# Performance work log

Hardware: AMD Instinct MI355X
Metric: run time of the kernel (lower is better)

The kernel has to match this reference:

```python
import jax, jax.numpy as jnp
import numpy as np

SL, BS, D = 2048, 2, 1024
H, DH = 16, 64  # num_heads, nhid

def setup_inputs() -> dict:
    key = jax.random.key(0)
    ks = jax.random.split(key, 8)
    inv = 1.0 / np.sqrt(D)
    return {
        "query": jax.random.normal(ks[0], (SL, BS, D), jnp.float32),
        "keys": jax.random.normal(ks[1], (SL, BS, D), jnp.float32),
        "values": jax.random.normal(ks[2], (SL, BS, D), jnp.float32),
        "mask": jnp.ones((1, 1, SL, SL), jnp.int32),
        "Wq": jax.random.normal(ks[3], (H * DH, D), jnp.float32) * inv,
        "Wk": jax.random.normal(ks[4], (H * DH, D), jnp.float32) * inv,
        "Wv": jax.random.normal(ks[5], (H * DH, D), jnp.float32) * inv,
        "Wo": jax.random.normal(ks[6], (D, H * DH), jnp.float32) * inv,
    }

def reference(query, keys, values, mask, Wq, Wk, Wv, Wo):
    slq, bs, _ = query.shape
    sl = keys.shape[0]
    # nn.Linear(bias=False): x @ W.T ; then view to (s, b, H, DH)
    q = (query @ Wq.T).reshape(slq, bs, H, DH)   # sbhd
    k = (keys @ Wk.T).reshape(sl, bs, H, DH)
    v = (values @ Wv.T).reshape(sl, bs, H, DH)
    # NOTE: original forward never applies self.scale -> unscaled scores.
    scores = jnp.einsum('qbhd,kbhd->bhqk', q, k)
    scores = jnp.where(mask == 0, jnp.float32(-1e20), scores)
    weights = jax.nn.softmax(scores, axis=-1)
    attn = jnp.einsum('bhqk,kbhd->qbhd', weights, v).reshape(slq, bs, H * DH)
    return attn @ Wo.T  # [slq, bs, out_dim]
```

## Files before the change

kernel.cpp:

```cpp
#include <hip/hip_runtime.h>


typedef __attribute__((ext_vector_type(4))) float  f32x4;
typedef __attribute__((ext_vector_type(8))) __bf16 bf16x8;
typedef __attribute__((ext_vector_type(4))) __bf16 bf16x4;

#define SLEN 2048
#define BSZ  2
#define DMODEL 1024
#define NHEAD 16
#define DHEAD 64
#define D3 (3 * DMODEL)

__device__ __forceinline__ void async16(void* lds, const void* g) {
    __builtin_amdgcn_global_load_lds(
        (const __attribute__((address_space(1))) unsigned int*)g,
        (__attribute__((address_space(3))) unsigned int*)lds, 16, 0, 0);
}

__device__ __forceinline__ f32x4 mfma16(bf16x8 a, bf16x8 b, f32x4 c) {
    return __builtin_amdgcn_mfma_f32_16x16x32_bf16(a, b, c, 0, 0, 0);
}

struct CvtArgs {
    const float* src[7];
    __bf16* dst[7];
    int n4[7];
    float scale[7];
    const int* mask;
    unsigned int* flag;
    int maskn4;
};
__global__ void cvt_all(CvtArgs a) {
    const int t = blockIdx.y;
    const int stride = gridDim.x * blockDim.x;
    if (t == 7) {
        bool ok = true;
        for (int i = blockIdx.x * blockDim.x + threadIdx.x; i < a.maskn4; i += stride) {
            int4 v = ((const int4*)a.mask)[i];
            ok = ok && v.x && v.y && v.z && v.w;
        }
        if (!ok) atomicAnd(a.flag, 0u);
        return;
    }
    const float* __restrict__ src = a.src[t];
    __bf16* __restrict__ dst = a.dst[t];
    const int n4 = a.n4[t];
    const float sc = a.scale[t];
    for (int i = blockIdx.x * blockDim.x + threadIdx.x; i < n4; i += stride) {
        float4 v = ((const float4*)src)[i];
        bf16x4 o;
        o[0] = (__bf16)(v.x * sc); o[1] = (__bf16)(v.y * sc);
        o[2] = (__bf16)(v.z * sc); o[3] = (__bf16)(v.w * sc);
        ((bf16x4*)dst)[i] = o;
    }
}

template <typename CT>
__device__ __forceinline__ void gemm_core(const char* Ab, const char* Bb, int K,
                                          CT* Cv, size_t crow0, size_t ccol0,
                                          size_t ldc) {
    __shared__ __bf16 At[2][128 * 64];
    __shared__ __bf16 Bt[2][64 * 64];
    const int tid = threadIdx.x;
    const int lane = tid & 63, wv = tid >> 6;
    const int l15 = lane & 15, l4 = lane >> 4;
    const int wr = wv >> 1, wc = wv & 1;
    const int srow = lane >> 3;
    const int sbyte = (((lane & 7) ^ srow) << 4);

    f32x4 acc[4][2];
#pragma unroll
    for (int m = 0; m < 4; m++)
#pragma unroll
        for (int n = 0; n < 2; n++)
#pragma unroll
            for (int r = 0; r < 4; r++) acc[m][n][r] = 0.0f;

    auto stage = [&](int buf, int k0) {
#pragma unroll
        for (int i = 0; i < 6; i++) {
            int c = wv * 6 + i;
            if (c < 16) {
                int row = c * 8 + srow;
                async16(&At[buf][c * 512], Ab + ((size_t)row * K + k0) * 2 + sbyte);
            } else {
                int row = (c - 16) * 8 + srow;
                async16(&Bt[buf][(c - 16) * 512], Bb + ((size_t)row * K + k0) * 2 + sbyte);
            }
        }
    };

    stage(0, 0);
    __syncthreads();
    int cur = 0;
    for (int k0 = 0; k0 < K; k0 += 64) {
        if (k0 + 64 < K) stage(cur ^ 1, k0 + 64);
#pragma unroll
        for (int kk = 0; kk < 2; kk++) {
            bf16x8 af[4], bfr[2];
#pragma unroll
            for (int m = 0; m < 4; m++) {
                int row = wr * 64 + m * 16 + l15;
                int col = (kk * 32 + l4 * 8) ^ ((row & 7) << 3);
                af[m] = *(const bf16x8*)&At[cur][row * 64 + col];
            }
#pragma unroll
            for (int n = 0; n < 2; n++) {
                int row = wc * 32 + n * 16 + l15;
                int col = (kk * 32 + l4 * 8) ^ ((row & 7) << 3);
                bfr[n] = *(const bf16x8*)&Bt[cur][row * 64 + col];
            }
#pragma unroll
            for (int m = 0; m < 4; m++)
#pragma unroll
                for (int n = 0; n < 2; n++)
                    acc[m][n] = mfma16(af[m], bfr[n], acc[m][n]);
        }
        __syncthreads();
        cur ^= 1;
    }

#pragma unroll
    for (int m = 0; m < 4; m++)
#pragma unroll
        for (int n = 0; n < 2; n++)
#pragma unroll
            for (int r = 0; r < 4; r++) {
                size_t row = crow0 + wr * 64 + m * 16 + l4 * 4 + r;
                size_t col = ccol0 + wc * 32 + n * 16 + l15;
                Cv[row * ldc + col] = (CT)acc[m][n][r];
            }
}

__global__ __launch_bounds__(256, 2) void gemm_qkv(const __bf16* __restrict__ Xq,
                                                   const __bf16* __restrict__ Xk,
                                                   const __bf16* __restrict__ Xv,
                                                   const __bf16* __restrict__ W,
                                                   __bf16* __restrict__ C) {
    const int i = blockIdx.x;
    const int swz = (i & 7) * 192 + (i >> 3);
    const int bn = swz / 32, bm = swz % 32;
    const __bf16* A = (bn < 16) ? Xq : (bn < 32) ? Xk : Xv;
    gemm_core<__bf16>((const char*)(A + (size_t)bm * 128 * DMODEL),
                      (const char*)(W + (size_t)bn * 64 * DMODEL), DMODEL,
                      C, (size_t)bm * 128, (size_t)bn * 64, D3);
}

__global__ __launch_bounds__(256, 2) void gemm_out(const __bf16* __restrict__ A,
                                                   const __bf16* __restrict__ B,
                                                   float* __restrict__ Cv) {
    const int i = blockIdx.x;
    const int swz = (i & 7) * 64 + (i >> 3);
    const int bn = swz / 32, bm = swz % 32;
    gemm_core<float>((const char*)(A + (size_t)bm * 128 * DMODEL),
                     (const char*)(B + (size_t)bn * 64 * DMODEL), DMODEL,
                     Cv, (size_t)bm * 128, (size_t)bn * 64, DMODEL);
}

__global__ __launch_bounds__(256) void transpose_v(const __bf16* __restrict__ QKV,
                                                   __bf16* __restrict__ Vt) {
    __shared__ __bf16 t[64][72];
    const int stile = blockIdx.x;
    const int bh = blockIdx.y;
    const int b = bh >> 4, h = bh & 15;
    const int tid = threadIdx.x;
    {
        int sr = tid >> 2, d0 = (tid & 3) * 16;
        const __bf16* src = QKV + ((size_t)((stile * 64 + sr) * BSZ + b) * D3 + 2 * DMODEL + h * 64 + d0);
        *(bf16x8*)&t[sr][d0]     = *(const bf16x8*)src;
        *(bf16x8*)&t[sr][d0 + 8] = *(const bf16x8*)(src + 8);
    }
    __syncthreads();
    {
        int d = tid >> 2, s0 = (tid & 3) * 16;
        bf16x8 o1, o2;
#pragma unroll
        for (int j = 0; j < 8; j++) { o1[j] = t[s0 + j][d]; o2[j] = t[s0 + 8 + j][d]; }
        __bf16* dst = Vt + ((size_t)(bh * 64 + d) * SLEN + stile * 64 + s0);
        *(bf16x8*)dst = o1;
        *(bf16x8*)(dst + 8) = o2;
    }
}

__global__ __launch_bounds__(256, 2) void attn_fwd(const __bf16* __restrict__ QKV,
                                                   const __bf16* __restrict__ Vt,
                                                   const int* __restrict__ mask,
                                                   const unsigned int* __restrict__ flag,
                                                   __bf16* __restrict__ Attn) {
    __shared__ __bf16 Kt[2][2][64 * 64];
    __shared__ __bf16 Vs[2][2][64 * 64];
    __shared__ __bf16 Ps[128 * 64];
    const int tid = threadIdx.x;
    const int lane = tid & 63, wv = tid >> 6;
    const int l15 = lane & 15, l4 = lane >> 4;
    const int blk = blockIdx.x;
    const int xcd = blk & 7, idx = blk >> 3;
    const int bh = xcd + (idx >> 4) * 8;
    const int qt = idx & 15;
    const int b = bh >> 4, h = bh & 15;
    const bool allones = (*flag != 0u);
    const int srow = lane >> 3;
    const int sbyte = (((lane & 7) ^ srow) << 4);

    bf16x8 aq[2][2];
#pragma unroll
    for (int m = 0; m < 2; m++)
#pragma unroll
        for (int kk = 0; kk < 2; kk++) {
            int qrow = qt * 128 + wv * 32 + m * 16 + l15;
            aq[m][kk] = *(const bf16x8*)(QKV + ((size_t)(qrow * BSZ + b) * D3 + h * 64 + kk * 32 + l4 * 8));
        }

    f32x4 o[2][4], lr[2];
#pragma unroll
    for (int m = 0; m < 2; m++) {
#pragma unroll
        for (int nd = 0; nd < 4; nd++)
#pragma unroll
            for (int r = 0; r < 4; r++) o[m][nd][r] = 0.0f;
#pragma unroll
        for (int r = 0; r < 4; r++) lr[m][r] = 0.0f;
    }

    const char* Kb = (const char*)QKV + ((size_t)b * D3 + DMODEL + h * 64) * 2;
    const char* Vb = (const char*)Vt + ((size_t)bh * 64) * SLEN * 2;

    auto stage = [&](int buf, int kt) {
#pragma unroll
        for (int i = 0; i < 8; i++) {
            int c = wv * 8 + i;
            if (c < 16) {
                int kh = c >> 3, ck = c & 7;
                int krow = kt * 128 + kh * 64 + ck * 8 + srow;
                async16(&Kt[buf][kh][ck * 512],
                        Kb + (size_t)krow * (BSZ * D3 * 2) + sbyte);
            } else {
                int c2 = c - 16;
                int kh = c2 >> 3, ck = c2 & 7;
                int drow = ck * 8 + srow;
                async16(&Vs[buf][kh][ck * 512],
                        Vb + (size_t)drow * (SLEN * 2) + kt * 256 + kh * 128 + sbyte);
            }
        }
    };

    stage(0, 0);
    __syncthreads();
    int cur = 0;

    for (int kt = 0; kt < SLEN / 128; kt++) {
        if (kt + 1 < SLEN / 128) stage(cur ^ 1, kt + 1);

#pragma unroll
        for (int kh = 0; kh < 2; kh++) {
            const __bf16* Kl = Kt[cur][kh];
            const __bf16* Vl = Vs[cur][kh];

            f32x4 s[2][4];
#pragma unroll
            for (int m = 0; m < 2; m++)
#pragma unroll
                for (int n = 0; n < 4; n++)
#pragma unroll
                    for (int r = 0; r < 4; r++) s[m][n][r] = 0.0f;
            __builtin_amdgcn_s_setprio(1);
#pragma unroll
            for (int n = 0; n < 4; n++) {
                int row = n * 16 + l15;
#pragma unroll
                for (int kk = 0; kk < 2; kk++) {
                    int col = (kk * 32 + l4 * 8) ^ ((row & 7) << 3);
                    bf16x8 bk = *(const bf16x8*)&Kl[row * 64 + col];
#pragma unroll
                    for (int m = 0; m < 2; m++)
                        s[m][n] = mfma16(aq[m][kk], bk, s[m][n]);
                }
            }
            __builtin_amdgcn_s_setprio(0);

            if (!allones) {
#pragma unroll
                for (int m = 0; m < 2; m++)
#pragma unroll
                    for (int n = 0; n < 4; n++)
#pragma unroll
                        for (int r = 0; r < 4; r++) {
                            int q = qt * 128 + wv * 32 + m * 16 + l4 * 4 + r;
                            int kg = kt * 128 + kh * 64 + n * 16 + l15;
                            if (mask[(size_t)q * SLEN + kg] == 0) s[m][n][r] = -1e20f;
                        }
            }

#pragma unroll
            for (int m = 0; m < 2; m++)
#pragma unroll
                for (int n = 0; n < 4; n++)
#pragma unroll
                    for (int r = 0; r < 4; r++) {
                        float p = __builtin_amdgcn_exp2f(s[m][n][r]);
                        lr[m][r] += p;
                        int row = wv * 32 + m * 16 + l4 * 4 + r;
                        int col = (n * 16 + l15) ^ ((row & 7) << 3);
                        Ps[row * 64 + col] = (__bf16)p;
                    }

            __builtin_amdgcn_s_setprio(1);
#pragma unroll
            for (int ks = 0; ks < 2; ks++) {
                bf16x8 ap[2];
#pragma unroll
                for (int m = 0; m < 2; m++) {
                    int prow = wv * 32 + m * 16 + l15;
                    int pcol = (ks * 32 + l4 * 8) ^ ((prow & 7) << 3);
                    ap[m] = *(const bf16x8*)&Ps[prow * 64 + pcol];
                }
#pragma unroll
                for (int nd = 0; nd < 4; nd++) {
                    int vrow = nd * 16 + l15;
                    int vcol = (ks * 32 + l4 * 8) ^ ((vrow & 7) << 3);
                    bf16x8 bv = *(const bf16x8*)&Vl[vrow * 64 + vcol];
#pragma unroll
                    for (int m = 0; m < 2; m++)
                        o[m][nd] = mfma16(ap[m], bv, o[m][nd]);
                }
            }
            __builtin_amdgcn_s_setprio(0);
        }

        __syncthreads();
        cur ^= 1;
    }

#pragma unroll
    for (int d = 1; d < 16; d <<= 1)
#pragma unroll
        for (int m = 0; m < 2; m++)
#pragma unroll
            for (int r = 0; r < 4; r++) lr[m][r] += __shfl_xor(lr[m][r], d);

#pragma unroll
    for (int m = 0; m < 2; m++) {
        f32x4 inv;
#pragma unroll
        for (int r = 0; r < 4; r++) inv[r] = 1.0f / lr[m][r];
#pragma unroll
        for (int nd = 0; nd < 4; nd++)
#pragma unroll
            for (int r = 0; r < 4; r++) {
                int qrow = qt * 128 + wv * 32 + m * 16 + l4 * 4 + r;
                Attn[((size_t)(qrow * BSZ + b)) * DMODEL + h * 64 + nd * 16 + l15] =
                    (__bf16)(o[m][nd][r] * inv[r]);
            }
    }
}

extern "C" void kernel_launch(void* const* d_in, const int* in_sizes, int n_in,
                              void* d_out, int out_size, void* d_ws, size_t ws_size,
                              hipStream_t stream) {
    const float* query  = (const float*)d_in[0];
    const float* keys   = (const float*)d_in[1];
    const float* values = (const float*)d_in[2];
    const int*   mask   = (const int*)d_in[3];
    const float* Wq     = (const float*)d_in[4];
    const float* Wk     = (const float*)d_in[5];
    const float* Wv     = (const float*)d_in[6];
    const float* Wo     = (const float*)d_in[7];
    float* out = (float*)d_out;

    char* ws = (char*)d_ws;
    const size_t MB = 1024 * 1024;
    __bf16* XQ   = (__bf16*)(ws + 0);
    __bf16* XK   = (__bf16*)(ws + 8 * MB);
    __bf16* XV   = (__bf16*)(ws + 16 * MB);
    __bf16* WCAT = (__bf16*)(ws + 24 * MB);
    __bf16* WQB  = WCAT;
    __bf16* WKB  = (__bf16*)(ws + 26 * MB);
    __bf16* WVB  = (__bf16*)(ws + 28 * MB);
    __bf16* WOB  = (__bf16*)(ws + 30 * MB);
    __bf16* QKV  = (__bf16*)(ws + 32 * MB);
    __bf16* VT   = (__bf16*)(ws + 0);
    __bf16* ATT  = (__bf16*)(ws + 8 * MB);
    unsigned int* flag = (unsigned int*)(ws + 56 * MB);

    (void)hipMemsetAsync(flag, 0xFF, 4, stream);

    const int NTOK = SLEN * BSZ;
    const int NBIG = NTOK * DMODEL / 4, NW = DMODEL * DMODEL / 4;
    const float LOG2E = 1.4426950408889634f;
    CvtArgs ca;
    ca.src[0] = query;  ca.dst[0] = XQ;  ca.n4[0] = NBIG; ca.scale[0] = 1.0f;
    ca.src[1] = keys;   ca.dst[1] = XK;  ca.n4[1] = NBIG; ca.scale[1] = 1.0f;
    ca.src[2] = values; ca.dst[2] = XV;  ca.n4[2] = NBIG; ca.scale[2] = 1.0f;
    ca.src[3] = Wq;     ca.dst[3] = WQB; ca.n4[3] = NW;   ca.scale[3] = LOG2E;
    ca.src[4] = Wk;     ca.dst[4] = WKB; ca.n4[4] = NW;   ca.scale[4] = 1.0f;
    ca.src[5] = Wv;     ca.dst[5] = WVB; ca.n4[5] = NW;   ca.scale[5] = 1.0f;
    ca.src[6] = Wo;     ca.dst[6] = WOB; ca.n4[6] = NW;   ca.scale[6] = 1.0f;
    ca.mask = mask; ca.flag = flag; ca.maskn4 = SLEN * SLEN / 4;
    cvt_all<<<dim3(256, 8), 256, 0, stream>>>(ca);

    gemm_qkv<<<1536, 256, 0, stream>>>(XQ, XK, XV, WCAT, QKV);

    transpose_v<<<dim3(SLEN / 64, BSZ * NHEAD), 256, 0, stream>>>(QKV, VT);

    attn_fwd<<<BSZ * NHEAD * (SLEN / 128), 256, 0, stream>>>(QKV, VT, mask, flag, ATT);

    gemm_out<<<512, 256, 0, stream>>>(ATT, WOB, out);
}
```

Before: 143.8 us.

## Keep softmax probabilities in registers via transposed QK^T and 16x16x16 MFMA for PV

The attention kernel swaps the QK^T MFMA operands so each lane holds scores for one query row across four keys. That lets the exp2 outputs feed a 16x16x16 bf16 MFMA directly as the B operand, so the shared-memory P buffer and its store/load round-trip are gone. Row-sum reductions shrink to two shuffles, output writes become 4-wide vectors, and K fragments are loaded up front. The change also drops the XCD-aware block swizzle in both GEMMs in favour of a plain 2D grid, which may hurt L2 locality. The PV product now issues twice as many smaller-K MFMAs.

```diff
diff --git a/kernel.cpp b/kernel.cpp
--- a/kernel.cpp
+++ b/kernel.cpp
@@ -4,6 +4,7 @@
 typedef __attribute__((ext_vector_type(4))) float  f32x4;
 typedef __attribute__((ext_vector_type(8))) __bf16 bf16x8;
 typedef __attribute__((ext_vector_type(4))) __bf16 bf16x4;
+typedef __attribute__((ext_vector_type(4))) short  s16x4;
 
 #define SLEN 2048
 #define BSZ  2
@@ -20,6 +21,15 @@
 
 __device__ __forceinline__ f32x4 mfma16(bf16x8 a, bf16x8 b, f32x4 c) {
     return __builtin_amdgcn_mfma_f32_16x16x32_bf16(a, b, c, 0, 0, 0);
+}
+
+__device__ __forceinline__ f32x4 mfma16k16(bf16x4 a, bf16x4 b, f32x4 c) {
+#if __has_builtin(__builtin_amdgcn_mfma_f32_16x16x16_bf16)
+    return __builtin_amdgcn_mfma_f32_16x16x16_bf16(a, b, c, 0, 0, 0);
+#else
+    return __builtin_amdgcn_mfma_f32_16x16x16bf16_1k(
+        __builtin_bit_cast(s16x4, a), __builtin_bit_cast(s16x4, b), c, 0, 0, 0);
+#endif
 }
 
 struct CvtArgs {
@@ -138,9 +148,7 @@
                                                    const __bf16* __restrict__ Xv,
                                                    const __bf16* __restrict__ W,
                                                    __bf16* __restrict__ C) {
-    const int i = blockIdx.x;
-    const int swz = (i & 7) * 192 + (i >> 3);
-    const int bn = swz / 32, bm = swz % 32;
+    const int bm = blockIdx.x, bn = blockIdx.y;
     const __bf16* A = (bn < 16) ? Xq : (bn < 32) ? Xk : Xv;
     gemm_core<__bf16>((const char*)(A + (size_t)bm * 128 * DMODEL),
                       (const char*)(W + (size_t)bn * 64 * DMODEL), DMODEL,
@@ -150,9 +158,7 @@
 __global__ __launch_bounds__(256, 2) void gemm_out(const __bf16* __restrict__ A,
                                                    const __bf16* __restrict__ B,
                                                    float* __restrict__ Cv) {
-    const int i = blockIdx.x;
-    const int swz = (i & 7) * 64 + (i >> 3);
-    const int bn = swz / 32, bm = swz % 32;
+    const int bm = blockIdx.x, bn = blockIdx.y;
     gemm_core<float>((const char*)(A + (size_t)bm * 128 * DMODEL),
                      (const char*)(B + (size_t)bn * 64 * DMODEL), DMODEL,
                      Cv, (size_t)bm * 128, (size_t)bn * 64, DMODEL);
@@ -190,7 +196,6 @@
                                                    __bf16* __restrict__ Attn) {
     __shared__ __bf16 Kt[2][2][64 * 64];
     __shared__ __bf16 Vs[2][2][64 * 64];
-    __shared__ __bf16 Ps[128 * 64];
     const int tid = threadIdx.x;
     const int lane = tid & 63, wv = tid >> 6;
     const int l15 = lane & 15, l4 = lane >> 4;
@@ -212,15 +217,15 @@
             aq[m][kk] = *(const bf16x8*)(QKV + ((size_t)(qrow * BSZ + b) * D3 + h * 64 + kk * 32 + l4 * 8));
         }
 
-    f32x4 o[2][4], lr[2];
+    f32x4 o[2][4];
+    float lr[2];
 #pragma unroll
     for (int m = 0; m < 2; m++) {
 #pragma unroll
         for (int nd = 0; nd < 4; nd++)
 #pragma unroll
             for (int r = 0; r < 4; r++) o[m][nd][r] = 0.0f;
-#pragma unroll
-        for (int r = 0; r < 4; r++) lr[m][r] = 0.0f;
+        lr[m] = 0.0f;
     }
 
     const char* Kb = (const char*)QKV + ((size_t)b * D3 + DMODEL + h * 64) * 2;
@@ -257,6 +262,17 @@
             const __bf16* Kl = Kt[cur][kh];
             const __bf16* Vl = Vs[cur][kh];
 
+            bf16x8 bk[4][2];
+#pragma unroll
+            for (int n = 0; n < 4; n++) {
+                int row = n * 16 + l15;
+#pragma unroll
+                for (int kk = 0; kk < 2; kk++) {
+                    int col = (kk * 32 + l4 * 8) ^ ((row & 7) << 3);
+                    bk[n][kk] = *(const bf16x8*)&Kl[row * 64 + col];
+                }
+            }
+
             f32x4 s[2][4];
 #pragma unroll
             for (int m = 0; m < 2; m++)
@@ -266,65 +282,63 @@
                     for (int r = 0; r < 4; r++) s[m][n][r] = 0.0f;
             __builtin_amdgcn_s_setprio(1);
 #pragma unroll
-            for (int n = 0; n < 4; n++) {
-                int row = n * 16 + l15;
-#pragma unroll
-                for (int kk = 0; kk < 2; kk++) {
-                    int col = (kk * 32 + l4 * 8) ^ ((row & 7) << 3);
-                    bf16x8 bk = *(const bf16x8*)&Kl[row * 64 + col];
+            for (int n = 0; n < 4; n++)
+#pragma unroll
+                for (int kk = 0; kk < 2; kk++)
 #pragma unroll
                     for (int m = 0; m < 2; m++)
-                        s[m][n] = mfma16(aq[m][kk], bk, s[m][n]);
-                }
-            }
+                        s[m][n] = mfma16(bk[n][kk], aq[m][kk], s[m][n]);
             __builtin_amdgcn_s_setprio(0);
 
             if (!allones) {
 #pragma unroll
-                for (int m = 0; m < 2; m++)
+                for (int m = 0; m < 2; m++) {
+                    int q = qt * 128 + wv * 32 + m * 16 + l15;
 #pragma unroll
                     for (int n = 0; n < 4; n++)
 #pragma unroll
                         for (int r = 0; r < 4; r++) {
-                            int q = qt * 128 + wv * 32 + m * 16 + l4 * 4 + r;
-                            int kg = kt * 128 + kh * 64 + n * 16 + l15;
+                            int kg = kt * 128 + kh * 64 + n * 16 + l4 * 4 + r;
                             if (mask[(size_t)q * SLEN + kg] == 0) s[m][n][r] = -1e20f;
                         }
-            }
-
+                }
+            }
+
+            bf16x4 pb[2][4];
 #pragma unroll
             for (int m = 0; m < 2; m++)
 #pragma unroll
-                for (int n = 0; n < 4; n++)
-#pragma unroll
-                    for (int r = 0; r < 4; r++) {
-                        float p = __builtin_amdgcn_exp2f(s[m][n][r]);
-                        lr[m][r] += p;
-                        int row = wv * 32 + m * 16 + l4 * 4 + r;
-                        int col = (n * 16 + l15) ^ ((row & 7) << 3);
-                        Ps[row * 64 + col] = (__bf16)p;
-                    }
+                for (int n = 0; n < 4; n++) {
+                    float p0 = __builtin_amdgcn_exp2f(s[m][n][0]);
+                    float p1 = __builtin_amdgcn_exp2f(s[m][n][1]);
+                    float p2 = __builtin_amdgcn_exp2f(s[m][n][2]);
+                    float p3 = __builtin_amdgcn_exp2f(s[m][n][3]);
+                    lr[m] += (p0 + p1) + (p2 + p3);
+                    bf16x4 w;
+                    w[0] = (__bf16)p0; w[1] = (__bf16)p1;
+                    w[2] = (__bf16)p2; w[3] = (__bf16)p3;
+                    pb[m][n] = w;
+                }
+
+            bf16x4 av[4][4];
+#pragma unroll
+            for (int nd = 0; nd < 4; nd++) {
+                int row = nd * 16 + l15;
+#pragma unroll
+                for (int n = 0; n < 4; n++) {
+                    int col = (n * 16 + l4 * 4) ^ ((row & 7) << 3);
+                    av[nd][n] = *(const bf16x4*)&Vl[row * 64 + col];
+                }
+            }
 
             __builtin_amdgcn_s_setprio(1);
 #pragma unroll
-            for (int ks = 0; ks < 2; ks++) {
-                bf16x8 ap[2];
-#pragma unroll
-                for (int m = 0; m < 2; m++) {
-                    int prow = wv * 32 + m * 16 + l15;
-                    int pcol = (ks * 32 + l4 * 8) ^ ((prow & 7) << 3);
-                    ap[m] = *(const bf16x8*)&Ps[prow * 64 + pcol];
-                }
-#pragma unroll
-                for (int nd = 0; nd < 4; nd++) {
-                    int vrow = nd * 16 + l15;
-                    int vcol = (ks * 32 + l4 * 8) ^ ((vrow & 7) << 3);
-                    bf16x8 bv = *(const bf16x8*)&Vl[vrow * 64 + vcol];
+            for (int n = 0; n < 4; n++)
+#pragma unroll
+                for (int nd = 0; nd < 4; nd++)
 #pragma unroll
                     for (int m = 0; m < 2; m++)
-                        o[m][nd] = mfma16(ap[m], bv, o[m][nd]);
-                }
-            }
+                        o[m][nd] = mfma16k16(av[nd][n], pb[m][n], o[m][nd]);
             __builtin_amdgcn_s_setprio(0);
         }
 
@@ -333,25 +347,22 @@
     }
 
 #pragma unroll
-    for (int d = 1; d < 16; d <<= 1)
-#pragma unroll
-        for (int m = 0; m < 2; m++)
-#pragma unroll
-            for (int r = 0; r < 4; r++) lr[m][r] += __shfl_xor(lr[m][r], d);
-
-#pragma unroll
     for (int m = 0; m < 2; m++) {
-        f32x4 inv;
-#pragma unroll
-        for (int r = 0; r < 4; r++) inv[r] = 1.0f / lr[m][r];
-#pragma unroll
-        for (int nd = 0; nd < 4; nd++)
-#pragma unroll
-            for (int r = 0; r < 4; r++) {
-                int qrow = qt * 128 + wv * 32 + m * 16 + l4 * 4 + r;
-                Attn[((size_t)(qrow * BSZ + b)) * DMODEL + h * 64 + nd * 16 + l15] =
-                    (__bf16)(o[m][nd][r] * inv[r]);
-            }
+        lr[m] += __shfl_xor(lr[m], 16);
+        lr[m] += __shfl_xor(lr[m], 32);
+    }
+
+#pragma unroll
+    for (int m = 0; m < 2; m++) {
+        float inv = 1.0f / lr[m];
+        int qrow = qt * 128 + wv * 32 + m * 16 + l15;
+#pragma unroll
+        for (int nd = 0; nd < 4; nd++) {
+            bf16x4 ov;
+#pragma unroll
+            for (int r = 0; r < 4; r++) ov[r] = (__bf16)(o[m][nd][r] * inv);
+            *(bf16x4*)(Attn + ((size_t)(qrow * BSZ + b)) * DMODEL + h * 64 + nd * 16 + l4 * 4) = ov;
+        }
     }
 }
 
@@ -399,11 +410,11 @@
     ca.mask = mask; ca.flag = flag; ca.maskn4 = SLEN * SLEN / 4;
     cvt_all<<<dim3(256, 8), 256, 0, stream>>>(ca);
 
-    gemm_qkv<<<1536, 256, 0, stream>>>(XQ, XK, XV, WCAT, QKV);
+    gemm_qkv<<<dim3(NTOK / 128, D3 / 64), 256, 0, stream>>>(XQ, XK, XV, WCAT, QKV);
 
     transpose_v<<<dim3(SLEN / 64, BSZ * NHEAD), 256, 0, stream>>>(QKV, VT);
 
     attn_fwd<<<BSZ * NHEAD * (SLEN / 128), 256, 0, stream>>>(QKV, VT, mask, flag, ATT);
 
-    gemm_out<<<512, 256, 0, stream>>>(ATT, WOB, out);
-}
+    gemm_out<<<dim3(NTOK / 128, DMODEL / 64), 256, 0, stream>>>(ATT, WOB, out);
+}
```

Result: faster. 135.8 us (-5.6%).
